# Kernel optimization log

Measured on AMD Instinct MI355X. Metric: run time of the kernel, lower is better.

Reference implementation:

```python
import jax, jax.numpy as jnp
import numpy as np

D_MODEL = 2048
D_INNER = 2048
N_QK = 32
N_V = 32
D_STATE = 64
D_CONV = 4
CHUNK = 128
CONV_DIM = D_INNER + 2 * N_QK * D_STATE  # 6144
IN_OUT = 2 * D_INNER + 2 * N_QK * D_STATE + N_V  # 8224


def setup_inputs() -> dict:
    key = jax.random.key(0)
    ks = jax.random.split(key, 6)
    u = jax.random.normal(ks[0], (2, 4096, D_MODEL), dtype=jnp.float32)
    W_in = jax.random.normal(ks[1], (IN_OUT, D_MODEL), dtype=jnp.float32) * 0.02
    conv_w = jax.random.normal(ks[2], (CONV_DIM, D_CONV), dtype=jnp.float32) * 0.2
    conv_b = jax.random.normal(ks[3], (CONV_DIM,), dtype=jnp.float32) * 0.02
    D = jnp.ones((N_V,), dtype=jnp.float32)
    z_bias = jnp.zeros((D_INNER,), dtype=jnp.float32)
    W_out = jax.random.normal(ks[4], (D_MODEL, D_INNER), dtype=jnp.float32) * 0.02
    return {"u": u, "W_in": W_in, "conv_w": conv_w, "conv_b": conv_b,
            "D": D, "z_bias": z_bias, "W_out": W_out}


def causal_depthwise_conv(x, w, b):
    # x: [B, L, C]; w: [C, K]; b: [C]. Torch Conv1d(groups=C, padding=K-1)[..., :L]
    B, L, C = x.shape
    K = w.shape[1]
    xp = jnp.pad(x, ((0, 0), (K - 1, 0), (0, 0)))
    y = b[None, None, :]
    for k in range(K):
        y = y + xp[:, k:k + L, :] * w[None, None, :, k]
    return y


def ssd_chunk_scan(x, dt, B, C, chunk):
    # Mamba2 SSD with A = -1 per head.
    # x: [b,l,h,p], dt: [b,l,h] (positive), B,C: [b,l,h,n]
    b, l, h, p = x.shape
    n = B.shape[-1]
    nc = l // chunk
    x = x.reshape(b, nc, chunk, h, p)
    dt = dt.reshape(b, nc, chunk, h)
    B = B.reshape(b, nc, chunk, h, n)
    C = C.reshape(b, nc, chunk, h, n)
    a = -dt                                  # A * dt
    cum = jnp.cumsum(a, axis=2)              # [b,nc,q,h]
    xdt = x * dt[..., None]                  # dt_t * x_t
    # ---- intra-chunk (causal, decay exp(cum_q - cum_k), q >= k) ----
    CB = jnp.einsum('bcqhn,bckhn->bchqk', C, B)
    cumT = jnp.swapaxes(cum, 2, 3)           # [b,nc,h,q]
    diff = cumT[..., :, None] - cumT[..., None, :]   # [b,nc,h,q,k]
    mask = jnp.tril(jnp.ones((chunk, chunk), dtype=bool))
    decay = jnp.exp(jnp.where(mask, diff, -jnp.inf))
    y_intra = jnp.einsum('bchqk,bckhp->bcqhp', CB * decay, xdt)
    # ---- per-chunk final states ----
    state_decay = jnp.exp(cum[:, :, -1:, :] - cum)   # [b,nc,q,h]
    states = jnp.einsum('bckhn,bckhp->bchpn', B * state_decay[..., None], xdt)
    chunk_decay = jnp.exp(cum[:, :, -1, :])          # [b,nc,h]
    # ---- inter-chunk recurrence ----
    def step(carry, inp):
        st, cd = inp  # st [b,h,p,n], cd [b,h]
        new = carry * cd[:, :, None, None] + st
        return new, carry  # emit the state *entering* this chunk
    init = jnp.zeros((b, h, p, n), dtype=x.dtype)
    _, prev = jax.lax.scan(step, init,
                           (jnp.moveaxis(states, 1, 0), jnp.moveaxis(chunk_decay, 1, 0)))
    prev = jnp.moveaxis(prev, 0, 1)                  # [b,nc,h,p,n]
    y_inter = jnp.einsum('bcqhn,bchpn->bcqhp', C * jnp.exp(cum)[..., None], prev)
    return (y_intra + y_inter).reshape(b, l, h, p)


def reference(u, W_in, conv_w, conv_b, D, z_bias, W_out):
    b, l, _ = u.shape  # l divisible by CHUNK (padded_len == l)
    xBCzA = jnp.einsum('bld,od->blo', u, W_in)
    xBC = xBCzA[..., :CONV_DIM]
    z = xBCzA[..., CONV_DIM:CONV_DIM + D_INNER]
    A_log = xBCzA[..., CONV_DIM + D_INNER:]
    xBC = causal_depthwise_conv(xBC, conv_w, conv_b)  # activation = identity
    x = xBC[..., :D_INNER]
    Bm = xBC[..., D_INNER:D_INNER + N_QK * D_STATE]
    Cm = xBC[..., D_INNER + N_QK * D_STATE:]
    x = x.reshape(b, l, N_V, D_INNER // N_V)
    Bm = Bm.reshape(b, l, N_QK, D_STATE)
    Cm = Cm.reshape(b, l, N_QK, D_STATE)
    dt = jax.nn.softplus(A_log)                       # [b,l,h]
    x_scan = x / dt[..., None]
    y = ssd_chunk_scan(x_scan, dt, Bm, Cm, CHUNK)
    y = y + D[None, None, :, None] * x                # Du uses undivided x
    y = y.reshape(b, l, D_INNER)
    out = jnp.einsum('bli,oi->blo', y * jax.nn.silu(z + z_bias), W_out)
    return out
```

## Files before the change

kernel.cpp:

```cpp
#include <hip/hip_runtime.h>
#include <math.h>

#define D_MODEL  2048
#define D_INNER  2048
#define N_QK     32
#define N_V      32
#define D_STATE  64
#define D_CONV   4
#define CHUNK    128
#define CONV_DIM 6144
#define IN_OUT   8224
#define BATCH    2
#define SEQ      4096
#define M_ROWS   (BATCH*SEQ)
#define NCHUNK   (SEQ/CHUNK)

typedef unsigned short bf16_t;
typedef __attribute__((ext_vector_type(4))) float f32x4;
typedef __attribute__((ext_vector_type(8))) short bf16x8;

#define SWZ64(r,c)  ((((r)*64)  + (c)) ^ (((r)&7)<<3))
#define SWZ128(r,c) ((((r)*128) + (c)) ^ (((r)&7)<<3))

__device__ __forceinline__ float b2f(bf16_t u) {
    union { unsigned int i; float f; } w; w.i = ((unsigned int)u) << 16; return w.f;
}
__device__ __forceinline__ bf16_t f2b(float f) {
    unsigned int x = __float_as_uint(f);
    return (bf16_t)((x + 0x7FFFu + ((x >> 16) & 1u)) >> 16);
}
__device__ __forceinline__ void store4b(bf16_t* dst, float4 v) {
    ushort4 u; u.x = f2b(v.x); u.y = f2b(v.y); u.z = f2b(v.z); u.w = f2b(v.w);
    *reinterpret_cast<ushort4*>(dst) = u;
}

__device__ __forceinline__ void gload_lds16(const bf16_t* g, bf16_t* l) {
    __builtin_amdgcn_global_load_lds((const __attribute__((address_space(1))) void*)g,
                                     (__attribute__((address_space(3))) void*)l,
                                     16, 0, 0);
}

__global__ __launch_bounds__(256) void f2b_kernel(const float* __restrict__ in,
                                                  bf16_t* __restrict__ out, long n)
{
    const long i = ((long)blockIdx.x * 256 + threadIdx.x) * 4;
    if (i < n) {
        float4 v = *reinterpret_cast<const float4*>(in + i);
        ushort4 o;
        o.x = f2b(v.x); o.y = f2b(v.y); o.z = f2b(v.z); o.w = f2b(v.w);
        *reinterpret_cast<ushort4*>(out + i) = o;
    }
}

template<int NTB, int K, bool OBF16, bool BNMAJOR>
__global__ __launch_bounds__(512, 2) void gemm256(const bf16_t* __restrict__ A,
                                                  const bf16_t* __restrict__ B,
                                                  void* __restrict__ Cv,
                                                  long ldc)
{
    constexpr int BK = 64;
    constexpr int NT = K / BK;
    __shared__ bf16_t As[2][2][8192];
    __shared__ bf16_t Bs[2][2][8192];

    const int nwg = gridDim.x;
    const int bid = blockIdx.x;
    const int wg  = ((nwg & 7) == 0) ? ((bid & 7) * (nwg >> 3) + (bid >> 3)) : bid;
    int bm, bn;
    if (BNMAJOR) { bm = (wg & 31) * 256; bn = (wg >> 5) * 256; }
    else         { bm = (wg / NTB) * 256; bn = (wg % NTB) * 256; }

    const int tid  = threadIdx.x;
    const int lane = tid & 63;
    const int wv   = tid >> 6;
    const int wr   = wv >> 2, wc = wv & 3;
    const int l15  = lane & 15, l4 = lane >> 4;

    f32x4 acc[8][4];
    #pragma unroll
    for (int i = 0; i < 8; ++i)
        #pragma unroll
        for (int j = 0; j < 4; ++j) acc[i][j] = (f32x4){0.f, 0.f, 0.f, 0.f};

    const bf16_t* Abase = A + (long)bm * K;
    const bf16_t* Bbase = B + (long)bn * K;

    auto stage_half = [&](int t, int buf, int kh) {
        #pragma unroll
        for (int it = 0; it < 2; ++it) {
            const int s   = it * 512 + tid;
            const int row = s >> 2;
            const int jp  = s & 3;
            const int jl  = jp ^ ((row >> 1) & 3);
            const long go = (long)row * K + t * BK + kh * 32 + jl * 8;
            gload_lds16(Abase + go, &As[buf][kh][s * 8]);
            gload_lds16(Bbase + go, &Bs[buf][kh][s * 8]);
        }
    };
    auto rdA = [&](int buf, int kh, int row) {
        const int jp = l4 ^ ((row >> 1) & 3);
        return *reinterpret_cast<const bf16x8*>(&As[buf][kh][(row * 4 + jp) * 8]);
    };
    auto rdB = [&](int buf, int kh, int row) {
        const int jp = l4 ^ ((row >> 1) & 3);
        return *reinterpret_cast<const bf16x8*>(&Bs[buf][kh][(row * 4 + jp) * 8]);
    };

    stage_half(0, 0, 0);
    stage_half(0, 0, 1);
    asm volatile("s_waitcnt vmcnt(4)" ::: "memory");
    __builtin_amdgcn_s_barrier();

    for (int t = 0; t < NT; ++t) {
        const int cur = t & 1;
        bf16x8 bfr[4], af[4];
        if (t + 1 < NT) stage_half(t + 1, cur ^ 1, 0);
        #pragma unroll
        for (int ni = 0; ni < 4; ++ni) bfr[ni] = rdB(cur, 0, wc * 64 + ni * 16 + l15);
        #pragma unroll
        for (int mi = 0; mi < 4; ++mi) af[mi] = rdA(cur, 0, wr * 128 + mi * 16 + l15);
        __builtin_amdgcn_s_setprio(1);
        #pragma unroll
        for (int mi = 0; mi < 4; ++mi)
            #pragma unroll
            for (int ni = 0; ni < 4; ++ni)
                acc[mi][ni] = __builtin_amdgcn_mfma_f32_16x16x32_bf16(
                    af[mi], bfr[ni], acc[mi][ni], 0, 0, 0);
        __builtin_amdgcn_s_setprio(0);
        __builtin_amdgcn_s_barrier();
        #pragma unroll
        for (int mi = 0; mi < 4; ++mi) af[mi] = rdA(cur, 0, wr * 128 + 64 + mi * 16 + l15);
        __builtin_amdgcn_s_setprio(1);
        #pragma unroll
        for (int mi = 0; mi < 4; ++mi)
            #pragma unroll
            for (int ni = 0; ni < 4; ++ni)
                acc[4 + mi][ni] = __builtin_amdgcn_mfma_f32_16x16x32_bf16(
                    af[mi], bfr[ni], acc[4 + mi][ni], 0, 0, 0);
        __builtin_amdgcn_s_setprio(0);
        if (t + 1 < NT) {
            stage_half(t + 1, cur ^ 1, 1);
            asm volatile("s_waitcnt vmcnt(8)" ::: "memory");
        } else {
            asm volatile("s_waitcnt vmcnt(0)" ::: "memory");
        }
        __builtin_amdgcn_s_barrier();
        #pragma unroll
        for (int ni = 0; ni < 4; ++ni) bfr[ni] = rdB(cur, 1, wc * 64 + ni * 16 + l15);
        #pragma unroll
        for (int mi = 0; mi < 4; ++mi) af[mi] = rdA(cur, 1, wr * 128 + mi * 16 + l15);
        __builtin_amdgcn_s_setprio(1);
        #pragma unroll
        for (int mi = 0; mi < 4; ++mi)
            #pragma unroll
            for (int ni = 0; ni < 4; ++ni)
                acc[mi][ni] = __builtin_amdgcn_mfma_f32_16x16x32_bf16(
                    af[mi], bfr[ni], acc[mi][ni], 0, 0, 0);
        __builtin_amdgcn_s_setprio(0);
        __builtin_amdgcn_s_barrier();
        #pragma unroll
        for (int mi = 0; mi < 4; ++mi) af[mi] = rdA(cur, 1, wr * 128 + 64 + mi * 16 + l15);
        __builtin_amdgcn_s_setprio(1);
        #pragma unroll
        for (int mi = 0; mi < 4; ++mi)
            #pragma unroll
            for (int ni = 0; ni < 4; ++ni)
                acc[4 + mi][ni] = __builtin_amdgcn_mfma_f32_16x16x32_bf16(
                    af[mi], bfr[ni], acc[4 + mi][ni], 0, 0, 0);
        __builtin_amdgcn_s_setprio(0);
        if (t + 1 < NT) { asm volatile("s_waitcnt vmcnt(4)" ::: "memory"); }
        __builtin_amdgcn_s_barrier();
    }

    #pragma unroll
    for (int mf = 0; mf < 8; ++mf) {
        const long grow0 = bm + wr * 128 + mf * 16 + l4 * 4;
        #pragma unroll
        for (int ni = 0; ni < 4; ++ni) {
            const int gcol = bn + wc * 64 + ni * 16 + l15;
            #pragma unroll
            for (int j = 0; j < 4; ++j) {
                if (OBF16)
                    ((bf16_t*)Cv)[(grow0 + j) * ldc + gcol] = f2b(acc[mf][ni][j]);
                else
                    ((float*)Cv)[(grow0 + j) * ldc + gcol] = acc[mf][ni][j];
            }
        }
    }
}

template<int N, int K, bool OBF16>
__global__ __launch_bounds__(256) void gemm_mfma(const bf16_t* __restrict__ A,
                                                 const bf16_t* __restrict__ B,
                                                 void* __restrict__ Cv,
                                                 long ldc)
{
    constexpr int BM = 128, BN = 128, BK = 64;
    constexpr int NTB = (N + BN - 1) / BN;
    __shared__ bf16_t As[BM * BK];
    __shared__ bf16_t Bs[BM * BK];

    const int nwg = gridDim.x;
    const int bid = blockIdx.x;
    const int wg  = ((nwg & 7) == 0) ? ((bid & 7) * (nwg >> 3) + (bid >> 3)) : bid;
    const int bm = (wg / NTB) * BM;
    const int bn = (wg % NTB) * BN;

    const int tid  = threadIdx.x;
    const int lane = tid & 63;
    const int wv   = tid >> 6;
    const int wr   = wv >> 1, wc = wv & 1;

    f32x4 acc[4][4];
    #pragma unroll
    for (int i = 0; i < 4; ++i)
        #pragma unroll
        for (int j = 0; j < 4; ++j) acc[i][j] = (f32x4){0.f, 0.f, 0.f, 0.f};

    for (int k0 = 0; k0 < K; k0 += BK) {
        #pragma unroll
        for (int it = 0; it < 4; ++it) {
            const int seg = it * 256 + tid;
            const int row = seg >> 3, c16 = seg & 7;
            gload_lds16(A + (long)(bm + row) * K + k0 + c16 * 8,
                        &As[row * BK + c16 * 8]);
            int brow = bn + row;
            if constexpr (N % BN != 0) brow = min(brow, N - 1);
            gload_lds16(B + (long)brow * K + k0 + c16 * 8,
                        &Bs[row * BK + c16 * 8]);
        }
        __syncthreads();
        #pragma unroll
        for (int kk = 0; kk < 2; ++kk) {
            bf16x8 af[4], bfr[4];
            const int kc = kk * 32 + (lane >> 4) * 8;
            #pragma unroll
            for (int mi = 0; mi < 4; ++mi) {
                const int row = wr * 64 + mi * 16 + (lane & 15);
                af[mi] = *reinterpret_cast<const bf16x8*>(&As[row * BK + kc]);
            }
            #pragma unroll
            for (int ni = 0; ni < 4; ++ni) {
                const int row = wc * 64 + ni * 16 + (lane & 15);
                bfr[ni] = *reinterpret_cast<const bf16x8*>(&Bs[row * BK + kc]);
            }
            #pragma unroll
            for (int mi = 0; mi < 4; ++mi)
                #pragma unroll
                for (int ni = 0; ni < 4; ++ni)
                    acc[mi][ni] = __builtin_amdgcn_mfma_f32_16x16x32_bf16(
                        af[mi], bfr[ni], acc[mi][ni], 0, 0, 0);
        }
        __syncthreads();
    }

    #pragma unroll
    for (int mi = 0; mi < 4; ++mi) {
        const long row0 = bm + wr * 64 + mi * 16 + ((lane >> 4) << 2);
        #pragma unroll
        for (int ni = 0; ni < 4; ++ni) {
            const int col = bn + wc * 64 + ni * 16 + (lane & 15);
            if (N % BN != 0 && col >= N) continue;
            #pragma unroll
            for (int j = 0; j < 4; ++j) {
                if (OBF16)
                    ((bf16_t*)Cv)[(row0 + j) * ldc + col] = f2b(acc[mi][ni][j]);
                else
                    ((float*)Cv)[(row0 + j) * ldc + col] = acc[mi][ni][j];
            }
        }
    }
}

__device__ __forceinline__ float4 conv4v(const bf16_t* __restrict__ xb, long m, int l,
                                         int col, const float* __restrict__ cw,
                                         const float* __restrict__ cbv)
{
    float4 acc = *reinterpret_cast<const float4*>(cbv + col);
    float4 wc0 = *reinterpret_cast<const float4*>(cw + (long)col * 4);
    float4 wc1 = *reinterpret_cast<const float4*>(cw + (long)col * 4 + 4);
    float4 wc2 = *reinterpret_cast<const float4*>(cw + (long)col * 4 + 8);
    float4 wc3 = *reinterpret_cast<const float4*>(cw + (long)col * 4 + 12);
    const float t0[4] = {wc0.x, wc0.y, wc0.z, wc0.w};
    const float t1[4] = {wc1.x, wc1.y, wc1.z, wc1.w};
    const float t2[4] = {wc2.x, wc2.y, wc2.z, wc2.w};
    const float t3[4] = {wc3.x, wc3.y, wc3.z, wc3.w};
    #pragma unroll
    for (int tap = 0; tap < 4; ++tap) {
        if (l - 3 + tap < 0) continue;
        const bf16_t* p = xb + (m - 3 + tap) * (long)IN_OUT + col;
        ushort4 v = *reinterpret_cast<const ushort4*>(p);
        acc.x = fmaf(b2f(v.x), t0[tap], acc.x);
        acc.y = fmaf(b2f(v.y), t1[tap], acc.y);
        acc.z = fmaf(b2f(v.z), t2[tap], acc.z);
        acc.w = fmaf(b2f(v.w), t3[tap], acc.w);
    }
    return acc;
}

__global__ __launch_bounds__(256) void ssd_states(const bf16_t* __restrict__ xb,
                                                  const float* __restrict__ cw,
                                                  const float* __restrict__ cbv,
                                                  bf16_t* __restrict__ states,
                                                  float* __restrict__ cumbuf,
                                                  float* __restrict__ cdecay)
{
    const int h = blockIdx.x, c = blockIdx.y, b = blockIdx.z;
    __shared__ bf16_t sx [128 * 64];
    __shared__ bf16_t sBr[128 * 64];
    __shared__ bf16_t sXT[64 * 128];
    __shared__ bf16_t sBT[64 * 128];
    __shared__ float  cum[CHUNK];
    __shared__ float  w0tot;
    const int t = threadIdx.x;
    const long mbase = (long)b * SEQ + (long)c * CHUNK;
    const long cb = ((long)b * NCHUNK + c) * N_QK + h;

    float v = 0.f;
    if (t < CHUNK) {
        const float a = b2f(xb[(mbase + t) * (long)IN_OUT + (CONV_DIM + D_INNER) + h]);
        v = -((a > 20.f) ? a : log1pf(expf(a)));
        #pragma unroll
        for (int s = 1; s < 64; s <<= 1) {
            const float u2 = __shfl_up(v, s, 64);
            if ((t & 63) >= s) v += u2;
        }
        if (t == 63) w0tot = v;
    }
    for (int idx = t; idx < CHUNK * 16; idx += 256) {
        const int k = idx >> 4, q4 = (idx & 15) * 4;
        const long m = mbase + k;
        const int l = (int)(m & (SEQ - 1));
        float4 xv = conv4v(xb, m, l, h * 64 + q4, cw, cbv);
        float4 bv = conv4v(xb, m, l, D_INNER + h * 64 + q4, cw, cbv);
        store4b(&sx [SWZ64(k, q4)], xv);
        store4b(&sBr[SWZ64(k, q4)], bv);
    }
    __syncthreads();
    if (t >= 64 && t < CHUNK) v += w0tot;
    if (t < CHUNK) cum[t] = v;
    __syncthreads();
    const float clast = cum[CHUNK - 1];
    {
        const int j = t & 127;
        const int c8b = (t >> 7) * 4;
        const float ej = __expf(clast - cum[j]);
        #pragma unroll
        for (int it = 0; it < 4; ++it) {
            const int c8 = c8b + it;
            bf16x8 xv = *reinterpret_cast<const bf16x8*>(&sx [SWZ64(j, c8 * 8)]);
            bf16x8 bv = *reinterpret_cast<const bf16x8*>(&sBr[SWZ64(j, c8 * 8)]);
            #pragma unroll
            for (int e = 0; e < 8; ++e) {
                sXT[SWZ128(c8 * 8 + e, j)] = xv[e];
                sBT[SWZ128(c8 * 8 + e, j)] = f2b(b2f((bf16_t)bv[e]) * ej);
            }
        }
    }
    __syncthreads();

    const int lane = t & 63, wv = t >> 6;
    const int l15 = lane & 15, l4 = lane >> 4;
    f32x4 acc[4];
    #pragma unroll
    for (int nj = 0; nj < 4; ++nj) acc[nj] = (f32x4){0.f, 0.f, 0.f, 0.f};
    #pragma unroll
    for (int ks = 0; ks < 4; ++ks) {
        const int kc = ks * 32 + l4 * 8;
        bf16x8 af = *reinterpret_cast<const bf16x8*>(&sXT[SWZ128(wv * 16 + l15, kc)]);
        #pragma unroll
        for (int nj = 0; nj < 4; ++nj) {
            bf16x8 bf = *reinterpret_cast<const bf16x8*>(&sBT[SWZ128(nj * 16 + l15, kc)]);
            acc[nj] = __builtin_amdgcn_mfma_f32_16x16x32_bf16(af, bf, acc[nj], 0, 0, 0);
        }
    }
    #pragma unroll
    for (int nj = 0; nj < 4; ++nj) {
        #pragma unroll
        for (int jj = 0; jj < 4; ++jj) {
            const int p = wv * 16 + l4 * 4 + jj;
            states[cb * 4096 + SWZ64(p, nj * 16 + l15)] = f2b(acc[nj][jj]);
        }
    }
    if (t < CHUNK) cumbuf[cb * CHUNK + t] = cum[t];
    if (t == 0)   cdecay[cb] = __expf(clast);
}

__global__ __launch_bounds__(256) void ssd_scan(bf16_t* __restrict__ states,
                                                const float* __restrict__ cdecay)
{
    const int bid = blockIdx.x;
    const int bh = bid >> 2, q = bid & 3;
    const int b = bh >> 5, h = bh & 31;
    const int t = threadIdx.x;
    const int off = q * 1024 + t * 4;
    float4 carry = make_float4(0.f, 0.f, 0.f, 0.f);
    for (int c = 0; c < NCHUNK; ++c) {
        const long cb = ((long)b * NCHUNK + c) * N_QK + h;
        bf16_t* p = states + cb * 4096 + off;
        const float cd = cdecay[cb];
        ushort4 su = *reinterpret_cast<const ushort4*>(p);
        ushort4 pv;
        pv.x = f2b(carry.x); pv.y = f2b(carry.y);
        pv.z = f2b(carry.z); pv.w = f2b(carry.w);
        *reinterpret_cast<ushort4*>(p) = pv;
        carry.x = fmaf(carry.x, cd, b2f(su.x));
        carry.y = fmaf(carry.y, cd, b2f(su.y));
        carry.z = fmaf(carry.z, cd, b2f(su.z));
        carry.w = fmaf(carry.w, cd, b2f(su.w));
    }
}

__global__ __launch_bounds__(256) void ssd_out(const bf16_t* __restrict__ xb,
                                               const float* __restrict__ cumbuf,
                                               const bf16_t* __restrict__ prevst,
                                               const float* __restrict__ Dvec,
                                               const float* __restrict__ zbias,
                                               const float* __restrict__ cw,
                                               const float* __restrict__ cbv,
                                               bf16_t* __restrict__ yz)
{
    const int h = blockIdx.x, c = blockIdx.y, b = blockIdx.z;
    __shared__ bf16_t sC[128 * 64];
    __shared__ bf16_t sB[128 * 64];
    __shared__ bf16_t sXQ[128 * 64];
    __shared__ bf16_t sXT[64 * 128];
    __shared__ bf16_t sP[64 * 64];
    __shared__ float  cum[CHUNK];
    const int t = threadIdx.x;
    const long mbase = (long)b * SEQ + (long)c * CHUNK;
    const long cb = ((long)b * NCHUNK + c) * N_QK + h;
    if (t < CHUNK) cum[t] = cumbuf[cb * CHUNK + t];
    #pragma unroll
    for (int it = 0; it < 2; ++it) {
        const int s = it * 256 + t;
        gload_lds16(prevst + cb * 4096 + s * 8, &sP[s * 8]);
    }
    for (int idx = t; idx < CHUNK * 16; idx += 256) {
        const int k = idx >> 4, q4 = (idx & 15) * 4;
        const long m = mbase + k;
        const int l = (int)(m & (SEQ - 1));
        float4 xv = conv4v(xb, m, l, h * 64 + q4, cw, cbv);
        float4 bv = conv4v(xb, m, l, D_INNER + h * 64 + q4, cw, cbv);
        float4 cv = conv4v(xb, m, l, 2 * D_INNER + h * 64 + q4, cw, cbv);
        store4b(&sXQ[SWZ64(k, q4)], xv);
        store4b(&sB [SWZ64(k, q4)], bv);
        store4b(&sC [SWZ64(k, q4)], cv);
    }
    __syncthreads();
    {
        const int j = t & 127;
        const int c8b = (t >> 7) * 4;
        #pragma unroll
        for (int it = 0; it < 4; ++it) {
            const int c8 = c8b + it;
            bf16x8 v = *reinterpret_cast<const bf16x8*>(&sXQ[SWZ64(j, c8 * 8)]);
            #pragma unroll
            for (int e = 0; e < 8; ++e) sXT[SWZ128(c8 * 8 + e, j)] = v[e];
        }
    }
    __syncthreads();

    const int lane = t & 63, wv = t >> 6;
    const int w32 = wv * 32, l15 = lane & 15, l4 = lane >> 4;
    bf16_t* sQ = sXQ;

    f32x4 yac[2][4], iac[2][4];
    #pragma unroll
    for (int mi = 0; mi < 2; ++mi)
        #pragma unroll
        for (int np = 0; np < 4; ++np) {
            yac[mi][np] = (f32x4){0.f, 0.f, 0.f, 0.f};
            iac[mi][np] = (f32x4){0.f, 0.f, 0.f, 0.f};
        }

    #pragma unroll
    for (int H = 0; H < 2; ++H) {
        if (H == 1 && wv < 2) break;
        const int j0 = H * 64;
        f32x4 sac[2][4];
        #pragma unroll
        for (int mi = 0; mi < 2; ++mi)
            #pragma unroll
            for (int nj = 0; nj < 4; ++nj) sac[mi][nj] = (f32x4){0.f, 0.f, 0.f, 0.f};
        #pragma unroll
        for (int kk = 0; kk < 2; ++kk) {
            const int kc = kk * 32 + l4 * 8;
            bf16x8 af0 = *reinterpret_cast<const bf16x8*>(&sC[SWZ64(w32 + l15, kc)]);
            bf16x8 af1 = *reinterpret_cast<const bf16x8*>(&sC[SWZ64(w32 + 16 + l15, kc)]);
            #pragma unroll
            for (int nj = 0; nj < 4; ++nj) {
                bf16x8 bfj = *reinterpret_cast<const bf16x8*>(&sB[SWZ64(j0 + nj * 16 + l15, kc)]);
                if (j0 + nj * 16 <= w32 + 15)
                    sac[0][nj] = __builtin_amdgcn_mfma_f32_16x16x32_bf16(af0, bfj, sac[0][nj], 0, 0, 0);
                if (j0 + nj * 16 <= w32 + 31)
                    sac[1][nj] = __builtin_amdgcn_mfma_f32_16x16x32_bf16(af1, bfj, sac[1][nj], 0, 0, 0);
            }
        }
        #pragma unroll
        for (int mi = 0; mi < 2; ++mi) {
            #pragma unroll
            for (int nj = 0; nj < 4; ++nj) {
                const int jcol = nj * 16 + l15;
                const int jg = j0 + jcol;
                #pragma unroll
                for (int jj = 0; jj < 4; ++jj) {
                    const int i = w32 + mi * 16 + l4 * 4 + jj;
                    const float q = (jg <= i) ? __expf(cum[i] - cum[jg]) * sac[mi][nj][jj] : 0.f;
                    sQ[SWZ64(i, jcol)] = f2b(q);
                }
            }
        }
        #pragma unroll
        for (int kk = 0; kk < 2; ++kk) {
            const int kc = kk * 32 + l4 * 8;
            bf16x8 qa0 = *reinterpret_cast<const bf16x8*>(&sQ[SWZ64(w32 + l15, kc)]);
            bf16x8 qa1 = *reinterpret_cast<const bf16x8*>(&sQ[SWZ64(w32 + 16 + l15, kc)]);
            #pragma unroll
            for (int np = 0; np < 4; ++np) {
                bf16x8 xf = *reinterpret_cast<const bf16x8*>(&sXT[SWZ128(np * 16 + l15, j0 + kc)]);
                yac[0][np] = __builtin_amdgcn_mfma_f32_16x16x32_bf16(qa0, xf, yac[0][np], 0, 0, 0);
                yac[1][np] = __builtin_amdgcn_mfma_f32_16x16x32_bf16(qa1, xf, yac[1][np], 0, 0, 0);
            }
        }
    }
    #pragma unroll
    for (int kk = 0; kk < 2; ++kk) {
        const int kc = kk * 32 + l4 * 8;
        bf16x8 cf0 = *reinterpret_cast<const bf16x8*>(&sC[SWZ64(w32 + l15, kc)]);
        bf16x8 cf1 = *reinterpret_cast<const bf16x8*>(&sC[SWZ64(w32 + 16 + l15, kc)]);
        #pragma unroll
        for (int np = 0; np < 4; ++np) {
            bf16x8 pf = *reinterpret_cast<const bf16x8*>(&sP[SWZ64(np * 16 + l15, kc)]);
            iac[0][np] = __builtin_amdgcn_mfma_f32_16x16x32_bf16(cf0, pf, iac[0][np], 0, 0, 0);
            iac[1][np] = __builtin_amdgcn_mfma_f32_16x16x32_bf16(cf1, pf, iac[1][np], 0, 0, 0);
        }
    }
    const float dh = Dvec[h];
    #pragma unroll
    for (int mi = 0; mi < 2; ++mi) {
        #pragma unroll
        for (int jj = 0; jj < 4; ++jj) {
            const int i = w32 + mi * 16 + l4 * 4 + jj;
            const float ei = __expf(cum[i]);
            const long m = mbase + i;
            const bf16_t* zr = xb + m * (long)IN_OUT + CONV_DIM + h * 64;
            bf16_t* orow = yz + m * (long)D_INNER + h * 64;
            #pragma unroll
            for (int np = 0; np < 4; ++np) {
                const int p = np * 16 + l15;
                const float xval = b2f(sXT[SWZ128(p, i)]);
                const float y = yac[mi][np][jj] + ei * iac[mi][np][jj] + dh * xval;
                const float zv = b2f(zr[p]) + zbias[h * 64 + p];
                const float s = zv / (1.f + __expf(-zv));
                orow[p] = f2b(y * s);
            }
        }
    }
}

extern "C" void kernel_launch(void* const* d_in, const int* in_sizes, int n_in,
                              void* d_out, int out_size, void* d_ws, size_t ws_size,
                              hipStream_t stream)
{
    const float* u      = (const float*)d_in[0];
    const float* W_in   = (const float*)d_in[1];
    const float* conv_w = (const float*)d_in[2];
    const float* conv_b = (const float*)d_in[3];
    const float* Dv     = (const float*)d_in[4];
    const float* z_bias = (const float*)d_in[5];
    const float* W_out  = (const float*)d_in[6];
    float* out = (float*)d_out;

    char* w = (char*)d_ws;
    bf16_t* xbcza = (bf16_t*)w;  w += (long)M_ROWS * IN_OUT * 2;
    bf16_t* wob   = (bf16_t*)w;  w += (long)2048 * 2048 * 2;
    char* ureg = w;
    bf16_t* ub  = (bf16_t*)ureg;
    bf16_t* wib = (bf16_t*)(ureg + (long)M_ROWS * D_MODEL * 2);
    bf16_t* yzb = (bf16_t*)ureg;
    float*  cumb   = (float*)(ureg + (long)M_ROWS * D_INNER * 2);
    bf16_t* states = (bf16_t*)(cumb + (long)BATCH * NCHUNK * N_QK * CHUNK);
    float*  cdec   = (float*)(states + (long)BATCH * NCHUNK * N_QK * 4096);

    f2b_kernel<<<(int)(((long)M_ROWS * D_MODEL / 4 + 255) / 256), 256, 0, stream>>>(
        u, ub, (long)M_ROWS * D_MODEL);
    f2b_kernel<<<(int)(((long)IN_OUT * D_MODEL / 4 + 255) / 256), 256, 0, stream>>>(
        W_in, wib, (long)IN_OUT * D_MODEL);
    f2b_kernel<<<(int)(((long)D_MODEL * D_INNER / 4 + 255) / 256), 256, 0, stream>>>(
        W_out, wob, (long)D_MODEL * D_INNER);

    gemm256<32, D_MODEL, true, true><<<(M_ROWS / 256) * 32, 512, 0, stream>>>(
        ub, wib, xbcza, IN_OUT);
    gemm_mfma<32, D_MODEL, true><<<(M_ROWS / 128), 256, 0, stream>>>(
        ub, wib + (long)8192 * D_MODEL, xbcza + 8192, IN_OUT);

    ssd_states<<<dim3(N_QK, NCHUNK, BATCH), 256, 0, stream>>>(xbcza, conv_w, conv_b,
                                                              states, cumb, cdec);

    ssd_scan<<<BATCH * N_QK * 4, 256, 0, stream>>>(states, cdec);

    ssd_out<<<dim3(N_QK, NCHUNK, BATCH), 256, 0, stream>>>(xbcza, cumb, states, Dv, z_bias,
                                                           conv_w, conv_b, yzb);

    gemm256<8, D_INNER, false, false><<<(M_ROWS / 256) * 8, 512, 0, stream>>>(
        yzb, wob, out, D_MODEL);
}
```

Baseline: 839.4 us.

## Cache conv'd X-transpose and B tiles from ssd_states for reuse in ssd_out

ssd_states now writes its already-convolved, transposed X tile and B tile to a workspace buffer, and ssd_out loads them with direct global-to-LDS copies. This replaces the recomputed depthwise conv and LDS transpose for X and B in ssd_out, when the workspace is large enough. The three f32-to-bf16 conversion launches are merged into one kernel. The first GEMM also drops its BN-major tile ordering for the default row-major ordering. The trade is extra global traffic (about 64MB written and read back) against the conv and transpose work, plus a change in GEMM cache locality.

```diff
diff --git a/kernel.cpp b/kernel.cpp
--- a/kernel.cpp
+++ b/kernel.cpp
@@ -40,19 +40,23 @@
                                      16, 0, 0);
 }
 
-__global__ __launch_bounds__(256) void f2b_kernel(const float* __restrict__ in,
-                                                  bf16_t* __restrict__ out, long n)
-{
-    const long i = ((long)blockIdx.x * 256 + threadIdx.x) * 4;
-    if (i < n) {
-        float4 v = *reinterpret_cast<const float4*>(in + i);
-        ushort4 o;
-        o.x = f2b(v.x); o.y = f2b(v.y); o.z = f2b(v.z); o.w = f2b(v.w);
-        *reinterpret_cast<ushort4*>(out + i) = o;
-    }
-}
-
-template<int NTB, int K, bool OBF16, bool BNMAJOR>
+__global__ __launch_bounds__(256) void f2b3_kernel(const float* __restrict__ a0, bf16_t* __restrict__ o0, long n0,
+                                                   const float* __restrict__ a1, bf16_t* __restrict__ o1, long n1,
+                                                   const float* __restrict__ a2, bf16_t* __restrict__ o2, long n2)
+{
+    long i = ((long)blockIdx.x * 256 + threadIdx.x) * 4;
+    const float* in; bf16_t* out;
+    if (i < n0)            { in = a0 + i; out = o0 + i; }
+    else if (i < n0 + n1)  { i -= n0; in = a1 + i; out = o1 + i; }
+    else if (i < n0 + n1 + n2) { i -= n0 + n1; in = a2 + i; out = o2 + i; }
+    else return;
+    float4 v = *reinterpret_cast<const float4*>(in);
+    ushort4 o;
+    o.x = f2b(v.x); o.y = f2b(v.y); o.z = f2b(v.z); o.w = f2b(v.w);
+    *reinterpret_cast<ushort4*>(out) = o;
+}
+
+template<int NTB, int K, bool OBF16>
 __global__ __launch_bounds__(512, 2) void gemm256(const bf16_t* __restrict__ A,
                                                   const bf16_t* __restrict__ B,
                                                   void* __restrict__ Cv,
@@ -66,9 +70,8 @@
     const int nwg = gridDim.x;
     const int bid = blockIdx.x;
     const int wg  = ((nwg & 7) == 0) ? ((bid & 7) * (nwg >> 3) + (bid >> 3)) : bid;
-    int bm, bn;
-    if (BNMAJOR) { bm = (wg & 31) * 256; bn = (wg >> 5) * 256; }
-    else         { bm = (wg / NTB) * 256; bn = (wg % NTB) * 256; }
+    const int bm = (wg / NTB) * 256;
+    const int bn = (wg % NTB) * 256;
 
     const int tid  = threadIdx.x;
     const int lane = tid & 63;
@@ -298,12 +301,15 @@
     return acc;
 }
 
+template<bool EXP>
 __global__ __launch_bounds__(256) void ssd_states(const bf16_t* __restrict__ xb,
                                                   const float* __restrict__ cw,
                                                   const float* __restrict__ cbv,
                                                   bf16_t* __restrict__ states,
                                                   float* __restrict__ cumbuf,
-                                                  float* __restrict__ cdecay)
+                                                  float* __restrict__ cdecay,
+                                                  bf16_t* __restrict__ xtg,
+                                                  bf16_t* __restrict__ bg)
 {
     const int h = blockIdx.x, c = blockIdx.y, b = blockIdx.z;
     __shared__ bf16_t sx [128 * 64];
@@ -380,6 +386,16 @@
         for (int jj = 0; jj < 4; ++jj) {
             const int p = wv * 16 + l4 * 4 + jj;
             states[cb * 4096 + SWZ64(p, nj * 16 + l15)] = f2b(acc[nj][jj]);
+        }
+    }
+    if constexpr (EXP) {
+        #pragma unroll
+        for (int it = 0; it < 4; ++it) {
+            const int s = it * 256 + t;
+            *reinterpret_cast<bf16x8*>(xtg + cb * 8192 + s * 8) =
+                *reinterpret_cast<const bf16x8*>(&sXT[s * 8]);
+            *reinterpret_cast<bf16x8*>(bg + cb * 8192 + s * 8) =
+                *reinterpret_cast<const bf16x8*>(&sBr[s * 8]);
         }
     }
     if (t < CHUNK) cumbuf[cb * CHUNK + t] = cum[t];
@@ -411,6 +427,7 @@
     }
 }
 
+template<bool EXP>
 __global__ __launch_bounds__(256) void ssd_out(const bf16_t* __restrict__ xb,
                                                const float* __restrict__ cumbuf,
                                                const bf16_t* __restrict__ prevst,
@@ -418,6 +435,8 @@
                                                const float* __restrict__ zbias,
                                                const float* __restrict__ cw,
                                                const float* __restrict__ cbv,
+                                               const bf16_t* __restrict__ xtg,
+                                               const bf16_t* __restrict__ bg,
                                                bf16_t* __restrict__ yz)
 {
     const int h = blockIdx.x, c = blockIdx.y, b = blockIdx.z;
@@ -436,30 +455,47 @@
         const int s = it * 256 + t;
         gload_lds16(prevst + cb * 4096 + s * 8, &sP[s * 8]);
     }
-    for (int idx = t; idx < CHUNK * 16; idx += 256) {
-        const int k = idx >> 4, q4 = (idx & 15) * 4;
-        const long m = mbase + k;
-        const int l = (int)(m & (SEQ - 1));
-        float4 xv = conv4v(xb, m, l, h * 64 + q4, cw, cbv);
-        float4 bv = conv4v(xb, m, l, D_INNER + h * 64 + q4, cw, cbv);
-        float4 cv = conv4v(xb, m, l, 2 * D_INNER + h * 64 + q4, cw, cbv);
-        store4b(&sXQ[SWZ64(k, q4)], xv);
-        store4b(&sB [SWZ64(k, q4)], bv);
-        store4b(&sC [SWZ64(k, q4)], cv);
-    }
-    __syncthreads();
-    {
-        const int j = t & 127;
-        const int c8b = (t >> 7) * 4;
+    if constexpr (EXP) {
         #pragma unroll
         for (int it = 0; it < 4; ++it) {
-            const int c8 = c8b + it;
-            bf16x8 v = *reinterpret_cast<const bf16x8*>(&sXQ[SWZ64(j, c8 * 8)]);
-            #pragma unroll
-            for (int e = 0; e < 8; ++e) sXT[SWZ128(c8 * 8 + e, j)] = v[e];
-        }
-    }
-    __syncthreads();
+            const int s = it * 256 + t;
+            gload_lds16(bg  + cb * 8192 + s * 8, &sB [s * 8]);
+            gload_lds16(xtg + cb * 8192 + s * 8, &sXT[s * 8]);
+        }
+        for (int idx = t; idx < CHUNK * 16; idx += 256) {
+            const int k = idx >> 4, q4 = (idx & 15) * 4;
+            const long m = mbase + k;
+            const int l = (int)(m & (SEQ - 1));
+            float4 cv = conv4v(xb, m, l, 2 * D_INNER + h * 64 + q4, cw, cbv);
+            store4b(&sC[SWZ64(k, q4)], cv);
+        }
+        __syncthreads();
+    } else {
+        for (int idx = t; idx < CHUNK * 16; idx += 256) {
+            const int k = idx >> 4, q4 = (idx & 15) * 4;
+            const long m = mbase + k;
+            const int l = (int)(m & (SEQ - 1));
+            float4 xv = conv4v(xb, m, l, h * 64 + q4, cw, cbv);
+            float4 bv = conv4v(xb, m, l, D_INNER + h * 64 + q4, cw, cbv);
+            float4 cv = conv4v(xb, m, l, 2 * D_INNER + h * 64 + q4, cw, cbv);
+            store4b(&sXQ[SWZ64(k, q4)], xv);
+            store4b(&sB [SWZ64(k, q4)], bv);
+            store4b(&sC [SWZ64(k, q4)], cv);
+        }
+        __syncthreads();
+        {
+            const int j = t & 127;
+            const int c8b = (t >> 7) * 4;
+            #pragma unroll
+            for (int it = 0; it < 4; ++it) {
+                const int c8 = c8b + it;
+                bf16x8 v = *reinterpret_cast<const bf16x8*>(&sXQ[SWZ64(j, c8 * 8)]);
+                #pragma unroll
+                for (int e = 0; e < 8; ++e) sXT[SWZ128(c8 * 8 + e, j)] = v[e];
+            }
+        }
+        __syncthreads();
+    }
 
     const int lane = t & 63, wv = t >> 6;
     const int w32 = wv * 32, l15 = lane & 15, l4 = lane >> 4;
@@ -575,34 +611,46 @@
     char* w = (char*)d_ws;
     bf16_t* xbcza = (bf16_t*)w;  w += (long)M_ROWS * IN_OUT * 2;
     bf16_t* wob   = (bf16_t*)w;  w += (long)2048 * 2048 * 2;
-    char* ureg = w;
+    char* ureg = w;  w += 67239936;
     bf16_t* ub  = (bf16_t*)ureg;
     bf16_t* wib = (bf16_t*)(ureg + (long)M_ROWS * D_MODEL * 2);
     bf16_t* yzb = (bf16_t*)ureg;
     float*  cumb   = (float*)(ureg + (long)M_ROWS * D_INNER * 2);
     bf16_t* states = (bf16_t*)(cumb + (long)BATCH * NCHUNK * N_QK * CHUNK);
     float*  cdec   = (float*)(states + (long)BATCH * NCHUNK * N_QK * 4096);
-
-    f2b_kernel<<<(int)(((long)M_ROWS * D_MODEL / 4 + 255) / 256), 256, 0, stream>>>(
-        u, ub, (long)M_ROWS * D_MODEL);
-    f2b_kernel<<<(int)(((long)IN_OUT * D_MODEL / 4 + 255) / 256), 256, 0, stream>>>(
-        W_in, wib, (long)IN_OUT * D_MODEL);
-    f2b_kernel<<<(int)(((long)D_MODEL * D_INNER / 4 + 255) / 256), 256, 0, stream>>>(
-        W_out, wob, (long)D_MODEL * D_INNER);
-
-    gemm256<32, D_MODEL, true, true><<<(M_ROWS / 256) * 32, 512, 0, stream>>>(
+    const long base_bytes = (long)(w - (char*)d_ws);
+    const long exp_bytes  = 2L * 2048 * 8192 * 2;
+    const bool use_exp = ((long)ws_size >= base_bytes + exp_bytes);
+    bf16_t* xtg = (bf16_t*)w;
+    bf16_t* bg  = xtg + (long)2048 * 8192;
+
+    {
+        const long n0 = (long)M_ROWS * D_MODEL;
+        const long n1 = (long)IN_OUT * D_MODEL;
+        const long n2 = (long)D_MODEL * D_INNER;
+        const long nb = ((n0 + n1 + n2) / 4 + 255) / 256;
+        f2b3_kernel<<<(int)nb, 256, 0, stream>>>(u, ub, n0, W_in, wib, n1, W_out, wob, n2);
+    }
+
+    gemm256<32, D_MODEL, true><<<(M_ROWS / 256) * 32, 512, 0, stream>>>(
         ub, wib, xbcza, IN_OUT);
     gemm_mfma<32, D_MODEL, true><<<(M_ROWS / 128), 256, 0, stream>>>(
         ub, wib + (long)8192 * D_MODEL, xbcza + 8192, IN_OUT);
 
-    ssd_states<<<dim3(N_QK, NCHUNK, BATCH), 256, 0, stream>>>(xbcza, conv_w, conv_b,
-                                                              states, cumb, cdec);
-
-    ssd_scan<<<BATCH * N_QK * 4, 256, 0, stream>>>(states, cdec);
-
-    ssd_out<<<dim3(N_QK, NCHUNK, BATCH), 256, 0, stream>>>(xbcza, cumb, states, Dv, z_bias,
-                                                           conv_w, conv_b, yzb);
-
-    gemm256<8, D_INNER, false, false><<<(M_ROWS / 256) * 8, 512, 0, stream>>>(
+    if (use_exp) {
+        ssd_states<true><<<dim3(N_QK, NCHUNK, BATCH), 256, 0, stream>>>(
+            xbcza, conv_w, conv_b, states, cumb, cdec, xtg, bg);
+        ssd_scan<<<BATCH * N_QK * 4, 256, 0, stream>>>(states, cdec);
+        ssd_out<true><<<dim3(N_QK, NCHUNK, BATCH), 256, 0, stream>>>(
+            xbcza, cumb, states, Dv, z_bias, conv_w, conv_b, xtg, bg, yzb);
+    } else {
+        ssd_states<false><<<dim3(N_QK, NCHUNK, BATCH), 256, 0, stream>>>(
+            xbcza, conv_w, conv_b, states, cumb, cdec, nullptr, nullptr);
+        ssd_scan<<<BATCH * N_QK * 4, 256, 0, stream>>>(states, cdec);
+        ssd_out<false><<<dim3(N_QK, NCHUNK, BATCH), 256, 0, stream>>>(
+            xbcza, cumb, states, Dv, z_bias, conv_w, conv_b, nullptr, nullptr, yzb);
+    }
+
+    gemm256<8, D_INNER, false><<<(M_ROWS / 256) * 8, 512, 0, stream>>>(
         yzb, wob, out, D_MODEL);
 }
```

New measurement: 824.4 us. About the same (-1.8%).
